# Performance work log

Hardware: AMD Instinct MI355X
Metric: run time of the kernel (lower is better)

## Reference

```python
import jax, jax.numpy as jnp
import numpy as np

N_NODES = 200000
N_EDGES = 6400000
HIDDEN = 200
N_HID_LAYERS = 6  # 8-layer MLP: in + 6 hidden + out


def setup_inputs() -> dict:
    key = jax.random.key(0)
    ks = jax.random.split(key, 12)
    x = jax.random.normal(ks[0], (N_NODES, 1), dtype=jnp.float32)
    edge_index = jax.random.randint(ks[1], (2, N_EDGES), 0, N_NODES, dtype=jnp.int64)
    # GraphConv(1,1): lin_rel (with bias) applied to aggregated neighbors, lin_root (no bias)
    w_rel = jax.random.normal(ks[2], (1, 1), dtype=jnp.float32)
    b_rel = jax.random.normal(ks[3], (1,), dtype=jnp.float32) * 0.1
    w_root = jax.random.normal(ks[4], (1, 1), dtype=jnp.float32)
    # MLP(1, 200, 1, num_layers=8)
    w_in = jax.random.normal(ks[5], (1, HIDDEN), dtype=jnp.float32) * (1.0 / 1.0)
    b_in = jnp.zeros((HIDDEN,), dtype=jnp.float32)
    w_hid = jax.random.normal(ks[6], (N_HID_LAYERS, HIDDEN, HIDDEN), dtype=jnp.float32) * (1.0 / np.sqrt(HIDDEN))
    b_hid = jnp.zeros((N_HID_LAYERS, HIDDEN), dtype=jnp.float32)
    w_out = jax.random.normal(ks[7], (HIDDEN, 1), dtype=jnp.float32) * (1.0 / np.sqrt(HIDDEN))
    b_out = jnp.zeros((1,), dtype=jnp.float32)
    return {
        "x": x, "edge_index": edge_index,
        "w_rel": w_rel, "b_rel": b_rel, "w_root": w_root,
        "w_in": w_in, "b_in": b_in,
        "w_hid": w_hid, "b_hid": b_hid,
        "w_out": w_out, "b_out": b_out,
    }


def reference(x, edge_index, w_rel, b_rel, w_root, w_in, b_in, w_hid, b_hid, w_out, b_out):
    # GraphConv with sum aggregation: out_i = W_rel @ sum_{j in N(i)} x_j + b_rel + W_root @ x_i
    src = edge_index[0]
    dst = edge_index[1]
    agg = jax.ops.segment_sum(x[src], dst, num_segments=N_NODES)  # [N, 1]
    h = agg @ w_rel + b_rel + x @ w_root                          # [N, 1]
    # 8-layer MLP with ReLU between layers
    h = jax.nn.relu(h @ w_in + b_in)                              # [N, 200]
    for i in range(N_HID_LAYERS):
        h = jax.nn.relu(h @ w_hid[i] + b_hid[i])
    h = h @ w_out + b_out                                         # [N, 1]
    return jax.nn.sigmoid(h)
```

## Files before the change

### kernel.cpp

```cpp
#include <hip/hip_runtime.h>

#define N_NODES 200000
#define N_EDGES 6400000
#define HID 200
#define NREP 8
#define MT 64

#define PK_ELEMS (7 * 14 * 512)
#define PK_HALF  (PK_ELEMS / 2)
#define STG_CHUNKS (PK_HALF * 2 / 16)

#define LDS_WOFF 28672
#define LDS_H0S  78848
#define LDS_TOTAL 79104

#define NPART 20
#define PNODES 10000
#define PBLK 50
#define CHUNK_E (N_EDGES / PBLK)
#define APPLY_LDS (PNODES * 4)

typedef float f32x4 __attribute__((ext_vector_type(4)));
typedef float f32x16 __attribute__((ext_vector_type(16)));
typedef _Float16 f16x8 __attribute__((ext_vector_type(8)));
typedef unsigned short u16;
typedef unsigned int u32;

__device__ __align__(16) float g_agg[N_NODES];
__device__ __align__(16) float g_xf8[NREP * N_NODES];
__device__ __align__(16) float g_wf[6 * HID * HID];
__device__ __align__(16) _Float16 g_wpk[6 * PK_ELEMS];
__device__ __align__(16) float g_ev[N_EDGES];
__device__ __align__(16) float g_part[NPART * PBLK * PNODES];
__device__ int g_isbf;

__device__ __forceinline__ float bf2f(u16 u) {
  union { u32 i; float f; } v; v.i = ((u32)u) << 16; return v.f;
}
__device__ __forceinline__ u16 f2bf(float f) {
  u32 i = __float_as_uint(f);
  return (u16)((i + 0x7FFFu + ((i >> 16) & 1u)) >> 16);
}
__device__ __forceinline__ float ldf(const void* p, int i, int isbf) {
  return isbf ? bf2f(((const u16*)p)[i]) : ((const float*)p)[i];
}
__device__ __forceinline__ void load_lds16(const void* g, void* l) {
  __builtin_amdgcn_global_load_lds(
      (const __attribute__((address_space(1))) u32*)g,
      (__attribute__((address_space(3))) u32*)l, 16, 0, 0);
}

constexpr int sf1(int m) { return (m & 7) + 1; }
constexpr int sf2(int m) { return ((m >> 3) & 3) + 2; }
constexpr int sg1(int k) { return (k & 7) + 1; }
constexpr int sg2(int k) { return ((k >> 3) & 1) + 1; }
constexpr int su1(int k) { return ((k * 3) & 7) + 1; }
constexpr int su2(int k) { return ((k >> 2) & 3) + 2; }
constexpr int sw1(int n) { return ((n * 5) & 7) + 1; }
constexpr int sw2(int n) { return ((n >> 3) & 3) + 1; }
constexpr int calcS32(int i, int j) {
  int s = 0;
  for (int k = 0; k < 16; ++k)
    s += (i ? sg2(k) : sg1(k)) * (j ? su2(k) : su1(k));
  return s;
}
__device__ __forceinline__ float refD32(int m, int n) {
  constexpr int S11 = calcS32(0, 0), S12 = calcS32(0, 1), S21 = calcS32(1, 0), S22 = calcS32(1, 1);
  return (float)(sf1(m) * sw1(n) * S11 + sf1(m) * sw2(n) * S12 +
                 sf2(m) * sw1(n) * S21 + sf2(m) * sw2(n) * S22);
}
__device__ int mfma_selftest32(int lane) {
  const int m = lane & 31, kh = lane >> 5;
  f16x8 av, bv;
#pragma unroll
  for (int j = 0; j < 8; ++j) {
    int k = kh * 8 + j;
    av[j] = (_Float16)(float)(sf1(m) * sg1(k) + sf2(m) * sg2(k));
    bv[j] = (_Float16)(float)(su1(k) * sw1(m) + su2(k) * sw2(m));
  }
  f32x16 z;
#pragma unroll
  for (int i = 0; i < 16; ++i) z[i] = 0.f;
  f32x16 d = __builtin_amdgcn_mfma_f32_32x32x16_f16(av, bv, z, 0, 0, 0);
  bool ok0 = true, ok1 = true;
#pragma unroll
  for (int reg = 0; reg < 16; ++reg) {
    int rr = (reg & 3) + 8 * (reg >> 2) + 4 * kh;
    ok0 = ok0 && (d[reg] == refD32(rr, m));
    ok1 = ok1 && (d[reg] == refD32(m, rr));
  }
  return __all(ok0) ? 0 : (__all(ok1) ? 1 : 2);
}

__global__ void sniff_kernel(const u32* __restrict__ xw) {
  int i = threadIdx.x;
  u32 e = (xw[i] >> 7) & 0xFFu;
  unsigned long long b = __ballot(e >= 110u && e <= 135u);
  if (i == 0) g_isbf = (__popcll(b) >= 48) ? 1 : 0;
}

__global__ void prep_kernel(const void* __restrict__ x, const void* __restrict__ w_hid) {
  int t = blockIdx.x * blockDim.x + threadIdx.x;
  int isbf = g_isbf;
  if (t < NREP * N_NODES) {
    int qd = t / N_NODES;
    int node = t - qd * N_NODES;
    g_xf8[t] = ldf(x, node, isbf);
  }
  if (t < 6 * HID * HID) g_wf[t] = ldf(w_hid, t, isbf);
  if (t < 6 * PK_ELEMS) {
    int l = t / PK_ELEMS;
    int r = t - l * PK_ELEMS;
    int h = r / PK_HALF;
    int r2 = r - h * PK_HALF;
    int tile = r2 / 3584;
    int r3 = r2 - tile * 3584;
    int ks7 = r3 >> 9;
    int r4 = r3 & 511;
    int ln = r4 >> 3;
    int j = r4 & 7;
    int n = tile * 32 + (ln & 31);
    int k = (h * 7 + ks7) * 16 + (ln >> 5) * 8 + j;
    float v = (n < HID && k < HID) ? ldf(w_hid, (l * HID + k) * HID + n, isbf) : 0.f;
    g_wpk[t] = (_Float16)v;
  }
}

__global__ void gather_kernel(const int* __restrict__ ei) {
  int t = blockIdx.x * blockDim.x + threadIdx.x;
  int e = t * 8;
  int xcc;
  asm volatile("s_getreg_b32 %0, hwreg(HW_REG_XCC_ID)" : "=s"(xcc));
  const float* xf = g_xf8 + (size_t)(xcc & (NREP - 1)) * N_NODES;
  bool is64 = ((ei[1] | ei[3] | ei[5] | ei[7]) == 0);
  int s[8];
  if (is64) {
#pragma unroll
    for (int i = 0; i < 4; ++i) {
      int4 a = *(const int4*)(ei + 2 * e + 4 * i);
      s[2 * i] = a.x; s[2 * i + 1] = a.z;
    }
  } else {
#pragma unroll
    for (int i = 0; i < 2; ++i) {
      int4 a = *(const int4*)(ei + e + 4 * i);
      s[4 * i] = a.x; s[4 * i + 1] = a.y; s[4 * i + 2] = a.z; s[4 * i + 3] = a.w;
    }
  }
  float v[8];
#pragma unroll
  for (int i = 0; i < 8; ++i) v[i] = xf[s[i]];
  *(float4*)(g_ev + e) = (float4){v[0], v[1], v[2], v[3]};
  *(float4*)(g_ev + e + 4) = (float4){v[4], v[5], v[6], v[7]};
}

__global__ __launch_bounds__(256) void apply_kernel(const int* __restrict__ ei) {
  extern __shared__ float part[];
  const int tid = threadIdx.x;
  const int p = blockIdx.x / PBLK;
  const int cb = blockIdx.x - p * PBLK;
  const int lo = p * PNODES;
  float4* pv = (float4*)part;
  for (int c = tid; c < PNODES / 4; c += 256) pv[c] = (float4){0.f, 0.f, 0.f, 0.f};
  __syncthreads();
  const bool is64 = ((ei[1] | ei[3] | ei[5] | ei[7]) == 0);
  const int base = cb * CHUNK_E;
  for (int g = 0; g < CHUNK_E / (256 * 4); ++g) {
    int idx = base + (g * 256 + tid) * 4;
    float4 v = *(const float4*)(g_ev + idx);
    int d0, d1, d2, d3;
    if (is64) {
      int4 b0 = *(const int4*)(ei + 2 * (size_t)N_EDGES + 2 * (size_t)idx);
      int4 b1 = *(const int4*)(ei + 2 * (size_t)N_EDGES + 2 * (size_t)idx + 4);
      d0 = b0.x; d1 = b0.z; d2 = b1.x; d3 = b1.z;
    } else {
      int4 b = *(const int4*)(ei + N_EDGES + idx);
      d0 = b.x; d1 = b.y; d2 = b.z; d3 = b.w;
    }
    unsigned u0 = (unsigned)(d0 - lo), u1 = (unsigned)(d1 - lo);
    unsigned u2 = (unsigned)(d2 - lo), u3 = (unsigned)(d3 - lo);
    if (u0 < PNODES) __hip_atomic_fetch_add(&part[u0], v.x, __ATOMIC_RELAXED, __HIP_MEMORY_SCOPE_WORKGROUP);
    if (u1 < PNODES) __hip_atomic_fetch_add(&part[u1], v.y, __ATOMIC_RELAXED, __HIP_MEMORY_SCOPE_WORKGROUP);
    if (u2 < PNODES) __hip_atomic_fetch_add(&part[u2], v.z, __ATOMIC_RELAXED, __HIP_MEMORY_SCOPE_WORKGROUP);
    if (u3 < PNODES) __hip_atomic_fetch_add(&part[u3], v.w, __ATOMIC_RELAXED, __HIP_MEMORY_SCOPE_WORKGROUP);
  }
  __syncthreads();
  float* gp = g_part + (size_t)blockIdx.x * PNODES;
  for (int c = tid; c < PNODES / 4; c += 256)
    *(float4*)(gp + c * 4) = pv[c];
}

__global__ void reduce_kernel() {
  int n = blockIdx.x * 256 + threadIdx.x;
  if (n >= N_NODES) return;
  int p = n / PNODES;
  int off = n - p * PNODES;
  const float* base = g_part + (size_t)p * PBLK * PNODES + off;
  float s = 0.f;
#pragma unroll
  for (int c = 0; c < PBLK; ++c) s += base[(size_t)c * PNODES];
  g_agg[n] = s;
}

__global__ __launch_bounds__(512, 4) void mlp_kernel(
    const void* __restrict__ w_rel, const void* __restrict__ b_rel, const void* __restrict__ w_root,
    const void* __restrict__ w_in, const void* __restrict__ b_in,
    const void* __restrict__ b_hid, const void* __restrict__ w_out, const void* __restrict__ b_out,
    void* __restrict__ out) {
  extern __shared__ char smem[];
  _Float16* actp = (_Float16*)smem;
  _Float16* wbuf = (_Float16*)(smem + LDS_WOFF);
  float* h0s = (float*)(smem + LDS_H0S);

  const int tid = threadIdx.x;
  const int nb = blockIdx.x * MT;
  const int isbf = g_isbf;
  const int lane = tid & 63;
  const int wv = tid >> 6;
  const int band = wv >> 2;
  const int cg = wv & 3;
  const int t0 = cg * 2;

  const int mode = mfma_selftest32(lane);

  if (tid < MT) {
    int node = nb + tid;
    h0s[tid] = g_agg[node] * ldf(w_rel, 0, isbf) + ldf(b_rel, 0, isbf) +
               g_xf8[node] * ldf(w_root, 0, isbf);
  }
  __syncthreads();

  if (mode < 2) {
    for (int u = tid; u < MT * 28; u += 512) {
      int m = u / 28, g = u - m * 28;
      int ks = g >> 1, kh = g & 1;
      float h0v = h0s[m];
      f16x8 pv;
#pragma unroll
      for (int j = 0; j < 8; ++j) {
        int col = ks * 16 + kh * 8 + j;
        float v = 0.f;
        if (col < HID) v = fmaxf(h0v * ldf(w_in, col, isbf) + ldf(b_in, col, isbf), 0.f);
        pv[j] = (_Float16)v;
      }
      *(f16x8*)(actp + ((m >> 5) * 14 + ks) * 512 + (kh * 32 + (m & 31)) * 8) = pv;
    }

    for (int l = 0; l < 6; ++l) {
      f32x16 acc0, acc1;
#pragma unroll
      for (int i = 0; i < 16; ++i) { acc0[i] = 0.f; acc1[i] = 0.f; }

#pragma unroll
      for (int h = 0; h < 2; ++h) {
        __syncthreads();
        {
          const _Float16* wg = g_wpk + (size_t)l * PK_ELEMS + h * PK_HALF;
          for (int c = tid; c < STG_CHUNKS; c += 512) load_lds16(wg + c * 8, wbuf + c * 8);
        }
        __syncthreads();

        f16x8 af[7];
#pragma unroll
        for (int i = 0; i < 7; ++i)
          af[i] = *(const f16x8*)(actp + (band * 14 + h * 7 + i) * 512 + lane * 8);

        if (cg < 3) {
#pragma unroll
          for (int i = 0; i < 7; ++i) {
            f16x8 b0 = *(const f16x8*)(wbuf + (t0 * 7 + i) * 512 + lane * 8);
            f16x8 b1 = *(const f16x8*)(wbuf + ((t0 + 1) * 7 + i) * 512 + lane * 8);
            acc0 = __builtin_amdgcn_mfma_f32_32x32x16_f16(af[i], b0, acc0, 0, 0, 0);
            acc1 = __builtin_amdgcn_mfma_f32_32x32x16_f16(af[i], b1, acc1, 0, 0, 0);
          }
        } else {
#pragma unroll
          for (int i = 0; i < 7; ++i) {
            f16x8 b0 = *(const f16x8*)(wbuf + (6 * 7 + i) * 512 + lane * 8);
            acc0 = __builtin_amdgcn_mfma_f32_32x32x16_f16(af[i], b0, acc0, 0, 0, 0);
          }
        }
      }
      __syncthreads();

      if (mode == 0) {
        const int c0 = lane & 31, kh = lane >> 5;
        {
          int col = t0 * 32 + c0;
          float bias = (col < HID) ? ldf(b_hid, l * HID + col, isbf) : 0.f;
          _Float16* dst = actp + (band * 14 + (col >> 4)) * 512 +
                          ((col >> 3) & 1) * 256 + (col & 7);
#pragma unroll
          for (int reg = 0; reg < 16; ++reg) {
            int rr = (reg & 3) + 8 * (reg >> 2) + 4 * kh;
            dst[rr * 8] = (_Float16)fmaxf(acc0[reg] + bias, 0.f);
          }
        }
        if (cg < 3) {
          int col = (t0 + 1) * 32 + c0;
          float bias = (col < HID) ? ldf(b_hid, l * HID + col, isbf) : 0.f;
          _Float16* dst = actp + (band * 14 + (col >> 4)) * 512 +
                          ((col >> 3) & 1) * 256 + (col & 7);
#pragma unroll
          for (int reg = 0; reg < 16; ++reg) {
            int rr = (reg & 3) + 8 * (reg >> 2) + 4 * kh;
            dst[rr * 8] = (_Float16)fmaxf(acc1[reg] + bias, 0.f);
          }
        }
      } else {
        const int rr = lane & 31, kh = lane >> 5;
#pragma unroll
        for (int reg = 0; reg < 16; ++reg) {
          int cc = (reg & 3) + 8 * (reg >> 2) + 4 * kh;
          {
            int col = t0 * 32 + cc;
            float v = acc0[reg] + ((col < HID) ? ldf(b_hid, l * HID + col, isbf) : 0.f);
            actp[(band * 14 + (col >> 4)) * 512 + (((col >> 3) & 1) * 32 + rr) * 8 + (col & 7)] =
                (_Float16)fmaxf(v, 0.f);
          }
          if (cg < 3) {
            int col = (t0 + 1) * 32 + cc;
            float v = acc1[reg] + ((col < HID) ? ldf(b_hid, l * HID + col, isbf) : 0.f);
            actp[(band * 14 + (col >> 4)) * 512 + (((col >> 3) & 1) * 32 + rr) * 8 + (col & 7)] =
                (_Float16)fmaxf(v, 0.f);
          }
        }
      }
    }

    __syncthreads();
    {
      int m = tid >> 3, c = tid & 7;
      const int mb = (m >> 5) * 14, ml = m & 31;
      float s = 0.f;
#pragma unroll
      for (int j = c * 25; j < c * 25 + 25; ++j) {
        _Float16 a = actp[(mb + (j >> 4)) * 512 + (((j >> 3) & 1) * 32 + ml) * 8 + (j & 7)];
        s += (float)a * ldf(w_out, j, isbf);
      }
      s += __shfl_down(s, 4);
      s += __shfl_down(s, 2);
      s += __shfl_down(s, 1);
      if (c == 0) {
        float logit = s + ldf(b_out, 0, isbf);
        float o = 1.f / (1.f + __expf(-logit));
        if (isbf) ((u16*)out)[nb + m] = f2bf(o);
        else ((float*)out)[nb + m] = o;
      }
    }
  } else {
    float(*fA)[201] = (float(*)[201])smem;
    float(*fB)[201] = (float(*)[201])(smem + 32 * 201 * 4);
    float* h0f = (float*)(smem + 64 * 201 * 4);
    for (int p = 0; p < 2; ++p) {
      __syncthreads();
      if (tid < 32) {
        int node = nb + p * 32 + tid;
        h0f[tid] = g_agg[node] * ldf(w_rel, 0, isbf) + ldf(b_rel, 0, isbf) +
                   g_xf8[node] * ldf(w_root, 0, isbf);
      }
      __syncthreads();
      for (int i = tid; i < 32 * HID; i += 512) {
        int mm = i / HID, ff = i - mm * HID;
        float v = h0f[mm] * ldf(w_in, ff, isbf) + ldf(b_in, ff, isbf);
        fA[mm][ff] = v > 0.f ? v : 0.f;
      }
      __syncthreads();
      const int m = tid >> 4, c = tid & 15;
      float(*ain)[201] = fA;
      float(*aout)[201] = fB;
      for (int l = 0; l < 6; ++l) {
        float acc[13];
#pragma unroll
        for (int jj = 0; jj < 13; ++jj) {
          int j = c * 13 + jj;
          acc[jj] = (j < HID) ? ldf(b_hid, l * HID + j, isbf) : 0.f;
        }
        const float* wl = g_wf + l * HID * HID;
        for (int k = 0; k < HID; ++k) {
          float a = ain[m][k];
          const float* wr = wl + k * HID;
#pragma unroll
          for (int jj = 0; jj < 13; ++jj) {
            int j = c * 13 + jj;
            if (j < HID) acc[jj] = fmaf(a, wr[j], acc[jj]);
          }
        }
        __syncthreads();
#pragma unroll
        for (int jj = 0; jj < 13; ++jj) {
          int j = c * 13 + jj;
          if (j < HID) aout[m][j] = fmaxf(acc[jj], 0.f);
        }
        float(*tsw)[201] = ain; ain = aout; aout = tsw;
        __syncthreads();
      }
      float s = 0.f;
      for (int j = c * 13; j < c * 13 + 13 && j < HID; ++j)
        s += ain[m][j] * ldf(w_out, j, isbf);
      s += __shfl_down(s, 8);
      s += __shfl_down(s, 4);
      s += __shfl_down(s, 2);
      s += __shfl_down(s, 1);
      int node = nb + p * 32 + m;
      if (c == 0) {
        float logit = s + ldf(b_out, 0, isbf);
        float o = 1.f / (1.f + __expf(-logit));
        if (isbf) ((u16*)out)[node] = f2bf(o);
        else ((float*)out)[node] = o;
      }
    }
  }
}

extern "C" void kernel_launch(void* const* d_in, const int* in_sizes, int n_in,
                              void* d_out, int out_size, void* d_ws, size_t ws_size,
                              hipStream_t stream) {
  const void* x      = d_in[0];
  const int* ei      = (const int*)d_in[1];
  const void* w_rel  = d_in[2];
  const void* b_rel  = d_in[3];
  const void* w_root = d_in[4];
  const void* w_in   = d_in[5];
  const void* b_in   = d_in[6];
  const void* w_hid  = d_in[7];
  const void* b_hid  = d_in[8];
  const void* w_out  = d_in[9];
  const void* b_out  = d_in[10];
  (void)d_ws; (void)ws_size; (void)in_sizes; (void)n_in; (void)out_size;

  sniff_kernel<<<1, 64, 0, stream>>>((const u32*)x);
  prep_kernel<<<(NREP * N_NODES + 255) / 256, 256, 0, stream>>>(x, w_hid);
  gather_kernel<<<N_EDGES / 8 / 256, 256, 0, stream>>>(ei);
  apply_kernel<<<NPART * PBLK, 256, APPLY_LDS, stream>>>(ei);
  reduce_kernel<<<(N_NODES + 255) / 256, 256, 0, stream>>>();
  mlp_kernel<<<N_NODES / MT, 512, LDS_TOTAL, stream>>>(
      w_rel, b_rel, w_root, w_in, b_in, b_hid, w_out, b_out, d_out);
}
```

Baseline: 589.9 us.

## Read MLP weights directly from global memory and pad activation LDS layout

Removes the per-layer LDS staging of packed fp16 weights (with its two barriers per half) and has each wave load its B fragments straight from global/L2. The activation tile layout is padded (528-element fragments, 264 offset) to reduce LDS bank conflicts, and hidden biases are preloaded into LDS once. The smaller LDS footprint allows more blocks per CU, but every wave now fetches weights separately from cache instead of sharing a staged copy.

```diff
diff --git a/kernel.cpp b/kernel.cpp
--- a/kernel.cpp
+++ b/kernel.cpp
@@ -8,11 +8,11 @@
 
 #define PK_ELEMS (7 * 14 * 512)
 #define PK_HALF  (PK_ELEMS / 2)
-#define STG_CHUNKS (PK_HALF * 2 / 16)
-
-#define LDS_WOFF 28672
-#define LDS_H0S  78848
-#define LDS_TOTAL 79104
+
+#define FR(band, ks) (((band) * 14 + (ks)) * 528)
+#define LDS_BIAS 29568
+#define LDS_H0S  34560
+#define LDS_TOTAL 51968
 
 #define NPART 20
 #define PNODES 10000
@@ -43,11 +43,6 @@
 }
 __device__ __forceinline__ float ldf(const void* p, int i, int isbf) {
   return isbf ? bf2f(((const u16*)p)[i]) : ((const float*)p)[i];
-}
-__device__ __forceinline__ void load_lds16(const void* g, void* l) {
-  __builtin_amdgcn_global_load_lds(
-      (const __attribute__((address_space(1))) u32*)g,
-      (__attribute__((address_space(3))) u32*)l, 16, 0, 0);
 }
 
 constexpr int sf1(int m) { return (m & 7) + 1; }
@@ -209,7 +204,7 @@
     void* __restrict__ out) {
   extern __shared__ char smem[];
   _Float16* actp = (_Float16*)smem;
-  _Float16* wbuf = (_Float16*)(smem + LDS_WOFF);
+  float* biasl = (float*)(smem + LDS_BIAS);
   float* h0s = (float*)(smem + LDS_H0S);
 
   const int tid = threadIdx.x;
@@ -220,6 +215,8 @@
   const int band = wv >> 2;
   const int cg = wv & 3;
   const int t0 = cg * 2;
+  const int m32 = lane & 31;
+  const int khl = lane >> 5;
 
   const int mode = mfma_selftest32(lane);
 
@@ -227,6 +224,10 @@
     int node = nb + tid;
     h0s[tid] = g_agg[node] * ldf(w_rel, 0, isbf) + ldf(b_rel, 0, isbf) +
                g_xf8[node] * ldf(w_root, 0, isbf);
+  }
+  for (int i = tid; i < 6 * 208; i += 512) {
+    int l = i / 208, c = i - l * 208;
+    biasl[i] = (c < HID) ? ldf(b_hid, l * HID + c, isbf) : 0.f;
   }
   __syncthreads();
 
@@ -243,8 +244,9 @@
         if (col < HID) v = fmaxf(h0v * ldf(w_in, col, isbf) + ldf(b_in, col, isbf), 0.f);
         pv[j] = (_Float16)v;
       }
-      *(f16x8*)(actp + ((m >> 5) * 14 + ks) * 512 + (kh * 32 + (m & 31)) * 8) = pv;
-    }
+      *(f16x8*)(actp + FR(m >> 5, ks) + kh * 264 + (m & 31) * 8) = pv;
+    }
+    __syncthreads();
 
     for (int l = 0; l < 6; ++l) {
       f32x16 acc0, acc1;
@@ -253,30 +255,23 @@
 
 #pragma unroll
       for (int h = 0; h < 2; ++h) {
-        __syncthreads();
-        {
-          const _Float16* wg = g_wpk + (size_t)l * PK_ELEMS + h * PK_HALF;
-          for (int c = tid; c < STG_CHUNKS; c += 512) load_lds16(wg + c * 8, wbuf + c * 8);
-        }
-        __syncthreads();
-
+        const _Float16* gb = g_wpk + (size_t)l * PK_ELEMS + h * PK_HALF + lane * 8;
         f16x8 af[7];
 #pragma unroll
         for (int i = 0; i < 7; ++i)
-          af[i] = *(const f16x8*)(actp + (band * 14 + h * 7 + i) * 512 + lane * 8);
-
+          af[i] = *(const f16x8*)(actp + FR(band, h * 7 + i) + khl * 264 + m32 * 8);
         if (cg < 3) {
 #pragma unroll
           for (int i = 0; i < 7; ++i) {
-            f16x8 b0 = *(const f16x8*)(wbuf + (t0 * 7 + i) * 512 + lane * 8);
-            f16x8 b1 = *(const f16x8*)(wbuf + ((t0 + 1) * 7 + i) * 512 + lane * 8);
+            f16x8 b0 = *(const f16x8*)(gb + (t0 * 7 + i) * 512);
+            f16x8 b1 = *(const f16x8*)(gb + ((t0 + 1) * 7 + i) * 512);
             acc0 = __builtin_amdgcn_mfma_f32_32x32x16_f16(af[i], b0, acc0, 0, 0, 0);
             acc1 = __builtin_amdgcn_mfma_f32_32x32x16_f16(af[i], b1, acc1, 0, 0, 0);
           }
         } else {
 #pragma unroll
           for (int i = 0; i < 7; ++i) {
-            f16x8 b0 = *(const f16x8*)(wbuf + (6 * 7 + i) * 512 + lane * 8);
+            f16x8 b0 = *(const f16x8*)(gb + (6 * 7 + i) * 512);
             acc0 = __builtin_amdgcn_mfma_f32_32x32x16_f16(af[i], b0, acc0, 0, 0, 0);
           }
         }
@@ -284,58 +279,53 @@
       __syncthreads();
 
       if (mode == 0) {
-        const int c0 = lane & 31, kh = lane >> 5;
         {
-          int col = t0 * 32 + c0;
-          float bias = (col < HID) ? ldf(b_hid, l * HID + col, isbf) : 0.f;
-          _Float16* dst = actp + (band * 14 + (col >> 4)) * 512 +
-                          ((col >> 3) & 1) * 256 + (col & 7);
+          int col = t0 * 32 + m32;
+          float bias = biasl[l * 208 + col];
+          _Float16* dst = actp + FR(band, col >> 4) + ((col >> 3) & 1) * 264 + (col & 7);
 #pragma unroll
           for (int reg = 0; reg < 16; ++reg) {
-            int rr = (reg & 3) + 8 * (reg >> 2) + 4 * kh;
+            int rr = (reg & 3) + 8 * (reg >> 2) + 4 * khl;
             dst[rr * 8] = (_Float16)fmaxf(acc0[reg] + bias, 0.f);
           }
         }
         if (cg < 3) {
-          int col = (t0 + 1) * 32 + c0;
-          float bias = (col < HID) ? ldf(b_hid, l * HID + col, isbf) : 0.f;
-          _Float16* dst = actp + (band * 14 + (col >> 4)) * 512 +
-                          ((col >> 3) & 1) * 256 + (col & 7);
+          int col = (t0 + 1) * 32 + m32;
+          float bias = biasl[l * 208 + col];
+          _Float16* dst = actp + FR(band, col >> 4) + ((col >> 3) & 1) * 264 + (col & 7);
 #pragma unroll
           for (int reg = 0; reg < 16; ++reg) {
-            int rr = (reg & 3) + 8 * (reg >> 2) + 4 * kh;
+            int rr = (reg & 3) + 8 * (reg >> 2) + 4 * khl;
             dst[rr * 8] = (_Float16)fmaxf(acc1[reg] + bias, 0.f);
           }
         }
       } else {
-        const int rr = lane & 31, kh = lane >> 5;
 #pragma unroll
         for (int reg = 0; reg < 16; ++reg) {
-          int cc = (reg & 3) + 8 * (reg >> 2) + 4 * kh;
+          int cc = (reg & 3) + 8 * (reg >> 2) + 4 * khl;
           {
             int col = t0 * 32 + cc;
-            float v = acc0[reg] + ((col < HID) ? ldf(b_hid, l * HID + col, isbf) : 0.f);
-            actp[(band * 14 + (col >> 4)) * 512 + (((col >> 3) & 1) * 32 + rr) * 8 + (col & 7)] =
+            float v = acc0[reg] + biasl[l * 208 + col];
+            actp[FR(band, col >> 4) + ((col >> 3) & 1) * 264 + m32 * 8 + (col & 7)] =
                 (_Float16)fmaxf(v, 0.f);
           }
           if (cg < 3) {
             int col = (t0 + 1) * 32 + cc;
-            float v = acc1[reg] + ((col < HID) ? ldf(b_hid, l * HID + col, isbf) : 0.f);
-            actp[(band * 14 + (col >> 4)) * 512 + (((col >> 3) & 1) * 32 + rr) * 8 + (col & 7)] =
+            float v = acc1[reg] + biasl[l * 208 + col];
+            actp[FR(band, col >> 4) + ((col >> 3) & 1) * 264 + m32 * 8 + (col & 7)] =
                 (_Float16)fmaxf(v, 0.f);
           }
         }
       }
-    }
-
-    __syncthreads();
+      __syncthreads();
+    }
+
     {
       int m = tid >> 3, c = tid & 7;
-      const int mb = (m >> 5) * 14, ml = m & 31;
       float s = 0.f;
 #pragma unroll
       for (int j = c * 25; j < c * 25 + 25; ++j) {
-        _Float16 a = actp[(mb + (j >> 4)) * 512 + (((j >> 3) & 1) * 32 + ml) * 8 + (j & 7)];
+        _Float16 a = actp[FR(m >> 5, j >> 4) + ((j >> 3) & 1) * 264 + (m & 31) * 8 + (j & 7)];
         s += (float)a * ldf(w_out, j, isbf);
       }
       s += __shfl_down(s, 4);
```

New measurement: 588.4 us. Within noise of the previous version (-0.3%).
